# Performance work log

Hardware: AMD Instinct MI355X
Metric: run time of the kernel (lower is better)

## Reference

```python
import jax, jax.numpy as jnp
import numpy as np

THRESHOLD = 0.3

def setup_inputs() -> dict:
    key = jax.random.key(0)
    ks = jax.random.split(key, 8)
    B, T, N, d = 4, 32, 1024, 2
    hd, od, hs, osz = 64, 64, 128, 2
    p = lambda k, sh: jax.random.normal(k, sh, jnp.float32) * 0.1
    return {
        "points": jax.random.uniform(ks[0], (B, T, N, d), jnp.float32),
        "W1": p(ks[1], (hd, d)),   "b1": jnp.zeros((hd,), jnp.float32),
        "W2": p(ks[2], (od, hd)),  "b2": jnp.zeros((od,), jnp.float32),
        "Wg": p(ks[3], (hd, od)),  "bg": jnp.zeros((hd,), jnp.float32),
        "Wih": p(ks[4], (3 * hs, hd)), "Whh": p(ks[5], (3 * hs, hs)),
        "bih": jnp.zeros((3 * hs,), jnp.float32), "bhh": jnp.zeros((3 * hs,), jnp.float32),
        "Wf": p(ks[6], (osz, hs)), "bf": jnp.zeros((osz,), jnp.float32),
    }

def _gcn_step(pts, W1, b1, W2, b2, Wg, bg):
    # pts: [N, d]. Torch detaches node features & adjacency (no grad to points).
    pts = jax.lax.stop_gradient(pts)
    dist = jnp.linalg.norm(pts[:, None, :] - pts[None, :, :], axis=2)  # [N,N]
    A = (dist < THRESHOLD).astype(pts.dtype)
    dinv = 1.0 / jnp.sqrt(A.sum(axis=1))          # rowsum >= 1 (self-loop)
    An = A * dinv[:, None] * dinv[None, :]        # D^{-1/2} A D^{-1/2}
    x = jax.nn.relu((An @ pts) @ W1.T + b1)       # [N, hd]
    x = jax.nn.relu((An @ x) @ W2.T + b2)         # [N, od]
    return x.mean(axis=0) @ Wg.T + bg             # [hd]

def reference(points, W1, b1, W2, b2, Wg, bg, Wih, Whh, bih, bhh, Wf, bf):
    # GCN per (batch, time): [B, T, hd]
    gcn = jax.vmap(jax.vmap(lambda p: _gcn_step(p, W1, b1, W2, b2, Wg, bg)))(points)
    H = Whh.shape[1]

    def gru_step(h, x):  # torch GRU gate order: r, z, n
        gi = x @ Wih.T + bih
        gh = h @ Whh.T + bhh
        ir, iz, inn = jnp.split(gi, 3)
        hr, hz, hn = jnp.split(gh, 3)
        r = jax.nn.sigmoid(ir + hr)
        z = jax.nn.sigmoid(iz + hz)
        n = jnp.tanh(inn + r * hn)
        h_new = (1.0 - z) * n + z * h
        return h_new, h_new

    h0 = jnp.zeros((H,), points.dtype)
    run = lambda xs: jax.lax.scan(gru_step, h0, xs)[1]   # [T, H]
    hs = jax.vmap(run)(gcn)                              # [B, T, H]
    y = hs @ Wf.T + bf                                   # [B, T, out]
    # torch: per-element gru_out.mean(dim=1, keepdim=True) on [1,T,out] -> [1,1,out], stacked -> [B,1,1,out]
    return y.mean(axis=1, keepdims=True)[:, :, None, :]
```

## Files before the change

### kernel.cpp

```cpp
#include <hip/hip_runtime.h>
#include <hip/hip_bf16.h>
#include <math.h>

#define N_PTS 1024
#define BT    128
typedef unsigned int u32;
typedef __attribute__((ext_vector_type(8))) short short8_t;
typedef __attribute__((ext_vector_type(4))) float f32x4;

__device__ __forceinline__ float bfi(u32 bits16) {
    union { u32 u; float f; } v; v.u = bits16 << 16; return v.f;
}
__device__ __forceinline__ unsigned short f2bf(float f) {
    union { float f; u32 u; } v; v.f = f;
    return (unsigned short)((v.u + 0x7FFFu + ((v.u >> 16) & 1u)) >> 16);
}
__device__ __forceinline__ float ldf(const void* p, int i, bool bf) {
    return bf ? bfi(((const unsigned short*)p)[i]) : ((const float*)p)[i];
}
__device__ __forceinline__ float2 ldp(const void* pbase, int j, bool bf) {
    if (bf) {
        u32 w = ((const u32*)pbase)[j];
        return make_float2(bfi(w & 0xFFFFu), bfi(w >> 16));
    }
    return ((const float2*)pbase)[j];
}
__device__ __forceinline__ bool detect_bf16(const void* pts, int tid, int* s_flag) {
    if (tid < 64) {
        u32 w = ((const u32*)pts)[tid];
        float v = bfi(w & 0xFFFFu);
        bool ok = (v >= 0.0f) && (v <= 1.0f);
        unsigned long long m = __ballot(ok);
        if (tid == 0) *s_flag = (m == 0xFFFFFFFFFFFFFFFFull) ? 1 : 0;
    }
    __syncthreads();
    return *s_flag != 0;
}
__device__ __forceinline__ bool is_nb(float px, float py, float qx, float qy) {
    float dx = px - qx, dy = py - qy;
    float d2 = __fadd_rn(__fmul_rn(dx, dx), __fmul_rn(dy, dy));
    return d2 < 0.09f;
}
__device__ __forceinline__ const void* pts_base(const void* pts, int bt, bool bf) {
    return bf ? (const void*)((const unsigned short*)pts + (size_t)bt * N_PTS * 2)
              : (const void*)((const float*)pts + (size_t)bt * N_PTS * 2);
}
__device__ __forceinline__ void gload16(const u32* g, u32* l) {
    __builtin_amdgcn_global_load_lds((const __attribute__((address_space(1))) u32*)g,
                                     (__attribute__((address_space(3))) u32*)l, 16, 0, 0);
}
__device__ __forceinline__ float rdlane(float v, int i) {
    return __int_as_float(__builtin_amdgcn_readlane(__float_as_int(v), i));
}
__device__ __forceinline__ float sigm_f(float x) {
    return __fdividef(1.0f, 1.0f + __expf(-x));
}
__device__ __forceinline__ float tanh_f(float x) {
    float e = __expf(2.0f * x);
    return 1.0f - __fdividef(2.0f, e + 1.0f);
}

__global__ __launch_bounds__(256) void k1_bm(const void* __restrict__ pts,
                                             float* __restrict__ dinv,
                                             float* __restrict__ gsum,
                                             u32* __restrict__ bm) {
    int blk = blockIdx.x, tid = threadIdx.x;
    int bt = blk >> 2, q = blk & 3;
    __shared__ float2 sp[N_PTS];
    __shared__ int s_flag;
    bool bf = detect_bf16(pts, tid, &s_flag);
    const void* pb = pts_base(pts, bt, bf);
    for (int j = tid; j < N_PTS; j += 256) sp[j] = ldp(pb, j, bf);
    if (blk < 32) gsum[blk * 256 + tid] = 0.0f;
    __syncthreads();
    int i = q * 256 + tid;
    float px = sp[i].x, py = sp[i].y;
    const float4* sp4 = (const float4*)sp;
    u32* bmrow = bm + (size_t)bt * 32768 + i;
    int cnt = 0;
    for (int c = 0; c < 32; c++) {
        u32 m = 0;
#pragma unroll
        for (int h = 0; h < 8; h++) {
            float4 s01 = sp4[c * 16 + 2 * h], s23 = sp4[c * 16 + 2 * h + 1];
            if (is_nb(px, py, s01.x, s01.y)) m |= 1u << (4 * h);
            if (is_nb(px, py, s01.z, s01.w)) m |= 1u << (4 * h + 1);
            if (is_nb(px, py, s23.x, s23.y)) m |= 1u << (4 * h + 2);
            if (is_nb(px, py, s23.z, s23.w)) m |= 1u << (4 * h + 3);
        }
        bmrow[c * 1024] = m;
        cnt += __popc(m);
    }
    dinv[bt * N_PTS + i] = 1.0f / sqrtf((float)cnt);
}

__global__ __launch_bounds__(256) void k2_x1v(const void* __restrict__ pts,
                                              const void* __restrict__ W1,
                                              const void* __restrict__ b1,
                                              const float* __restrict__ dinv,
                                              const u32* __restrict__ bm,
                                              u32* __restrict__ x1vB) {
    int blk = blockIdx.x, tid = threadIdx.x;
    int bt = blk >> 2, q = blk & 3;
    __shared__ u32 sbm[8192];
    __shared__ unsigned short u_lds[4][1032];
    __shared__ float2 sax[256];
    __shared__ float  sdl[256];
    __shared__ int s_flag;
    bool bf = detect_bf16(pts, tid, &s_flag);
    const void* pb = pts_base(pts, bt, bf);
    for (int j = tid; j < N_PTS; j += 256) {
        float2 p = ldp(pb, j, bf);
        float d = dinv[bt * N_PTS + j];
        float ux = d * p.x, uy = d * p.y;
        unsigned short hx = f2bf(ux), hy = f2bf(uy);
        u_lds[0][j] = hx;
        u_lds[1][j] = hy;
        u_lds[2][j] = f2bf(ux - bfi(hx));
        u_lds[3][j] = f2bf(uy - bfi(hy));
    }
    const u32* bg_ = bm + (size_t)bt * 32768 + q * 256;
    for (int idx = tid; idx < 8192; idx += 256) {
        int c = idx >> 8, r = idx & 255;
        sbm[idx] = bg_[c * 1024 + r];
    }
    sdl[tid] = dinv[bt * N_PTS + q * 256 + tid];
    __syncthreads();

    int lane = tid & 63, w = tid >> 6;
    int l15 = lane & 15, quad = lane >> 4;
    f32x4 acc[4];
#pragma unroll
    for (int rf = 0; rf < 4; rf++)
#pragma unroll
        for (int r = 0; r < 4; r++) acc[rf][r] = 0.0f;

    const unsigned short* urow = &u_lds[l15 & 3][0];
    for (int c = 0; c < 32; c++) {
        short8_t bu = *(const short8_t*)(urow + c * 32 + quad * 8);
#pragma unroll
        for (int rf = 0; rf < 4; rf++) {
            u32 mw = sbm[c * 256 + w * 64 + rf * 16 + l15];
            u32 by = (mw >> (quad * 8)) & 0xFFu;
            short8_t v;
#pragma unroll
            for (int i2 = 0; i2 < 8; i2++)
                v[i2] = (by & (1u << i2)) ? (short)0x3F80 : (short)0;
            acc[rf] = __builtin_amdgcn_mfma_f32_16x16x32_bf16(v, bu, acc[rf], 0, 0, 0);
        }
    }
#pragma unroll
    for (int rf = 0; rf < 4; rf++) {
#pragma unroll
        for (int r = 0; r < 4; r++) {
            float vsum = acc[rf][r] + __shfl_xor(acc[rf][r], 2, 64);
            int row = w * 64 + rf * 16 + quad * 4 + r;
            float sc = vsum * sdl[row];
            if (l15 == 0)      sax[row].x = sc;
            else if (l15 == 1) sax[row].y = sc;
        }
    }
    __syncthreads();
    int ch = tid & 63, wq = tid >> 6;
    float w0 = ldf(W1, 2 * ch, bf), w1v = ldf(W1, 2 * ch + 1, bf), bb = ldf(b1, ch, bf);
    for (int tt = 0; tt < 4; tt++) {
        u32 ow[8];
#pragma unroll
        for (int k2i = 0; k2i < 8; k2i++) {
            int lj = tt * 64 + wq * 16 + 2 * k2i;
            float2 a0 = sax[lj], a1 = sax[lj + 1];
            float v0 = sdl[lj]     * fmaxf(fmaf(w0, a0.x, fmaf(w1v, a0.y, bb)), 0.0f);
            float v1 = sdl[lj + 1] * fmaxf(fmaf(w0, a1.x, fmaf(w1v, a1.y, bb)), 0.0f);
            ow[k2i] = (u32)f2bf(v0) | ((u32)f2bf(v1) << 16);
        }
        u32* dst = x1vB + ((size_t)(bt * 16 + q * 4 + tt) * 64 + ch) * 36 + wq * 8;
        *(uint4*)dst = make_uint4(ow[0], ow[1], ow[2], ow[3]);
        *(uint4*)(dst + 4) = make_uint4(ow[4], ow[5], ow[6], ow[7]);
    }
}

__global__ __launch_bounds__(256) void k3_mfma(const void* __restrict__ pts,
                                               const void* __restrict__ W2,
                                               const void* __restrict__ b2,
                                               const float* __restrict__ dinv,
                                               const u32* __restrict__ bm,
                                               const u32* __restrict__ x1vB,
                                               float* __restrict__ gsum) {
    __shared__ u32 pool[15424];
    __shared__ int s_flag;
    float* poolf = (float*)pool;
    int tid = threadIdx.x, lane = tid & 63, w = tid >> 6;
    int l15 = lane & 15, quad = lane >> 4;
    int blk = blockIdx.x, bt = blk & 127, rowblk = blk >> 7;
    bool bf = detect_bf16(pts, tid, &s_flag);

    const u32* xg = x1vB + (size_t)bt * 36864;
    for (int it = w; it < 9; it += 4)
        gload16(xg + it * 256 + lane * 4, pool + 8192 + it * 256 + lane * 4);

    const u32* bg_ = bm + (size_t)bt * 32768 + rowblk * 256;
    for (int idx = tid; idx < 8192; idx += 256) {
        int c = idx >> 8, r = idx & 255;
        pool[idx] = bg_[c * 1024 + r];
    }
    unsigned short* W2B = (unsigned short*)(pool + 12800);
    for (int idx = tid; idx < 4096; idx += 256) {
        int o = idx >> 6, c = idx & 63;
        W2B[o * 72 + c] = f2bf(ldf(W2, idx, bf));
    }
    if (tid < 256) poolf[15104 + tid] = dinv[bt * N_PTS + rowblk * 256 + tid];
    if (tid < 64)  poolf[15360 + tid] = ldf(b2, tid, bf);

    f32x4 acc[4][4];
#pragma unroll
    for (int rf = 0; rf < 4; rf++)
#pragma unroll
        for (int nb = 0; nb < 4; nb++)
#pragma unroll
            for (int r = 0; r < 4; r++) acc[rf][nb][r] = 0.0f;

    for (int t = 0; t < 16; t++) {
        __syncthreads();
        if (t + 1 < 16) {
            u32* dst = pool + ((t & 1) ? 8192 : 10496);
            const u32* src = xg + (t + 1) * 2304;
            for (int it = w; it < 9; it += 4)
                gload16(src + it * 256 + lane * 4, dst + it * 256 + lane * 4);
        }
        const unsigned short* xf = (const unsigned short*)(pool + ((t & 1) ? 10496 : 8192));
#pragma unroll
        for (int ks = 0; ks < 2; ks++) {
            short8_t bq[4];
#pragma unroll
            for (int rf = 0; rf < 4; rf++) {
                u32 mw = pool[(2 * t + ks) * 256 + w * 64 + rf * 16 + l15];
                u32 by = (mw >> (quad * 8)) & 0xFFu;
                short8_t v;
#pragma unroll
                for (int i2 = 0; i2 < 8; i2++)
                    v[i2] = (by & (1u << i2)) ? (short)0x3F80 : (short)0;
                bq[rf] = v;
            }
#pragma unroll
            for (int nb = 0; nb < 4; nb++) {
                short8_t af = *(const short8_t*)(xf + (nb * 16 + l15) * 72 + ks * 32 + quad * 8);
#pragma unroll
                for (int rf = 0; rf < 4; rf++)
                    acc[rf][nb] = __builtin_amdgcn_mfma_f32_16x16x32_bf16(af, bq[rf], acc[rf][nb], 0, 0, 0);
            }
        }
    }
    __syncthreads();

    u32* dump = pool;
#pragma unroll
    for (int rf = 0; rf < 4; rf++) {
        int rn = w * 64 + rf * 16 + l15;
        float di = poolf[15104 + rn];
#pragma unroll
        for (int nb = 0; nb < 4; nb++) {
            u32 lo = (u32)f2bf(acc[rf][nb][0] * di) | ((u32)f2bf(acc[rf][nb][1] * di) << 16);
            u32 hi = (u32)f2bf(acc[rf][nb][2] * di) | ((u32)f2bf(acc[rf][nb][3] * di) << 16);
            u32* dst = dump + rn * 36 + nb * 8 + quad * 2;
            dst[0] = lo; dst[1] = hi;
        }
    }
    __syncthreads();
    f32x4 xacc[4][4];
#pragma unroll
    for (int ob = 0; ob < 4; ob++)
#pragma unroll
        for (int rf = 0; rf < 4; rf++)
#pragma unroll
            for (int r = 0; r < 4; r++) xacc[ob][rf][r] = 0.0f;
#pragma unroll
    for (int ks2 = 0; ks2 < 2; ks2++) {
        short8_t b2f[4];
#pragma unroll
        for (int rf = 0; rf < 4; rf++)
            b2f[rf] = *(const short8_t*)((const unsigned short*)dump +
                        (w * 64 + rf * 16 + l15) * 72 + ks2 * 32 + quad * 8);
#pragma unroll
        for (int ob = 0; ob < 4; ob++) {
            short8_t a2 = *(const short8_t*)(W2B + (ob * 16 + l15) * 72 + ks2 * 32 + quad * 8);
#pragma unroll
            for (int rf = 0; rf < 4; rf++)
                xacc[ob][rf] = __builtin_amdgcn_mfma_f32_16x16x32_bf16(a2, b2f[rf], xacc[ob][rf], 0, 0, 0);
        }
    }
#pragma unroll
    for (int ob = 0; ob < 4; ob++) {
#pragma unroll
        for (int r = 0; r < 4; r++) {
            int o = ob * 16 + quad * 4 + r;
            float bb = poolf[15360 + o];
            float s = 0.0f;
#pragma unroll
            for (int rf = 0; rf < 4; rf++) s += fmaxf(xacc[ob][rf][r] + bb, 0.0f);
            s += __shfl_down(s, 8, 16);
            s += __shfl_down(s, 4, 16);
            s += __shfl_down(s, 2, 16);
            s += __shfl_down(s, 1, 16);
            if (l15 == 0) atomicAdd(&gsum[bt * 64 + o], s);
        }
    }
}

__global__ __launch_bounds__(384, 1) void k4a_gi(const void* __restrict__ pts,
                                                 const void* __restrict__ Wg,
                                                 const void* __restrict__ bg,
                                                 const void* __restrict__ Wih,
                                                 const void* __restrict__ bih,
                                                 const float* __restrict__ gsum,
                                                 float* __restrict__ gi_ws) {
    int blk = blockIdx.x, tid = threadIdx.x;
    __shared__ float s_gm[64];
    __shared__ float s_x[64];
    __shared__ int s_flag;
    bool bf = detect_bf16(pts, tid, &s_flag);
    if (tid < 64) s_gm[tid] = gsum[(size_t)blk * 64 + tid] * (1.0f / 1024.0f);
    int r = tid;
    float wv[64];
    if (bf) {
#pragma unroll
        for (int k = 0; k < 64; k++) wv[k] = bfi(((const unsigned short*)Wih)[r * 64 + k]);
    } else {
        const float4* wr = (const float4*)Wih + r * 16;
#pragma unroll
        for (int qq = 0; qq < 16; qq++) {
            float4 v = wr[qq];
            wv[4*qq] = v.x; wv[4*qq+1] = v.y; wv[4*qq+2] = v.z; wv[4*qq+3] = v.w;
        }
    }
    float br = ldf(bih, r, bf);
    float wg[64];
    if (tid < 64) {
        if (bf) {
#pragma unroll
            for (int k = 0; k < 64; k++) wg[k] = bfi(((const unsigned short*)Wg)[tid * 64 + k]);
        } else {
            const float4* wr = (const float4*)Wg + tid * 16;
#pragma unroll
            for (int qq = 0; qq < 16; qq++) {
                float4 v = wr[qq];
                wg[4*qq] = v.x; wg[4*qq+1] = v.y; wg[4*qq+2] = v.z; wg[4*qq+3] = v.w;
            }
        }
    }
    __syncthreads();
    if (tid < 64) {
        float gmv = s_gm[tid];
        float s0 = ldf(bg, tid, bf), s1 = 0.f, s2 = 0.f, s3 = 0.f;
#pragma unroll
        for (int k = 0; k < 64; k += 4) {
            s0 = fmaf(wg[k],     rdlane(gmv, k),     s0);
            s1 = fmaf(wg[k + 1], rdlane(gmv, k + 1), s1);
            s2 = fmaf(wg[k + 2], rdlane(gmv, k + 2), s2);
            s3 = fmaf(wg[k + 3], rdlane(gmv, k + 3), s3);
        }
        s_x[tid] = (s0 + s1) + (s2 + s3);
    }
    __syncthreads();
    float xv = s_x[tid & 63];
    float s0 = br, s1 = 0.f, s2 = 0.f, s3 = 0.f;
#pragma unroll
    for (int k = 0; k < 64; k += 4) {
        s0 = fmaf(wv[k],     rdlane(xv, k),     s0);
        s1 = fmaf(wv[k + 1], rdlane(xv, k + 1), s1);
        s2 = fmaf(wv[k + 2], rdlane(xv, k + 2), s2);
        s3 = fmaf(wv[k + 3], rdlane(xv, k + 3), s3);
    }
    gi_ws[(size_t)blk * 384 + r] = (s0 + s1) + (s2 + s3);
}

__global__ __launch_bounds__(768, 1) void k4b_scan(const void* __restrict__ pts,
                                                   const void* __restrict__ Whh,
                                                   const void* __restrict__ bhh,
                                                   const void* __restrict__ Wf,
                                                   const void* __restrict__ bf_,
                                                   const float* __restrict__ gi_ws,
                                                   float* __restrict__ out) {
    int b = blockIdx.x, tid = threadIdx.x;
    __shared__ float s_gi[12288];
    __shared__ float s_part[2][768];
    __shared__ float s_hm[128];
    __shared__ int s_flag;
    bool bf = detect_bf16(pts, tid, &s_flag);
    const u32* gi_g = (const u32*)gi_ws + (size_t)b * 12288;
    u32* s_gi_u = (u32*)s_gi;
#pragma unroll
    for (int j = 0; j < 4; j++)
        gload16(gi_g + j * 3072 + tid * 4, s_gi_u + j * 3072 + tid * 4);

    int hi = (tid >= 384) ? 1 : 0;
    int r = tid - hi * 384;
    int lane = tid & 63;
    float wh2[64];
    {
        int koff = hi * 64;
        if (bf) {
#pragma unroll
            for (int k = 0; k < 64; k++)
                wh2[k] = bfi(((const unsigned short*)Whh)[r * 128 + koff + k]);
        } else {
            const float4* wr = (const float4*)Whh + (r * 128 + koff) / 4;
#pragma unroll
            for (int qq = 0; qq < 16; qq++) {
                float4 v = wr[qq];
                wh2[4*qq] = v.x; wh2[4*qq+1] = v.y; wh2[4*qq+2] = v.z; wh2[4*qq+3] = v.w;
            }
        }
    }
    float bhr = hi ? 0.0f : ldf(bhh, r, bf);
    int c = hi * 64 + lane;
    float hval = 0.0f;
    float hsum = 0.0f;
    __syncthreads();

    for (int t = 0; t < 32; t++) {
        float gi_r = s_gi[t * 384 + c];
        float gi_z = s_gi[t * 384 + 128 + c];
        float gi_n = s_gi[t * 384 + 256 + c];
        float s0 = bhr, s1 = 0.f, s2 = 0.f, s3 = 0.f;
#pragma unroll
        for (int k = 0; k < 64; k += 4) {
            s0 = fmaf(wh2[k],     rdlane(hval, k),     s0);
            s1 = fmaf(wh2[k + 1], rdlane(hval, k + 1), s1);
            s2 = fmaf(wh2[k + 2], rdlane(hval, k + 2), s2);
            s3 = fmaf(wh2[k + 3], rdlane(hval, k + 3), s3);
        }
        s_part[t & 1][tid] = (s0 + s1) + (s2 + s3);
        __syncthreads();
        const float* P = s_part[t & 1];
        float gr = gi_r + P[c]       + P[384 + c];
        float gz = gi_z + P[128 + c] + P[512 + c];
        float hn =        P[256 + c] + P[640 + c];
        float rr = sigm_f(gr);
        float z  = sigm_f(gz);
        float n  = tanh_f(fmaf(rr, hn, gi_n));
        hval = fmaf(z, hval - n, n);
        hsum += hval;
    }
    if (tid < 64) s_hm[tid] = hsum * (1.0f / 32.0f);
    else if (tid >= 384 && tid < 448) s_hm[64 + lane] = hsum * (1.0f / 32.0f);
    __syncthreads();
    if (tid < 128) {
        float hm = s_hm[tid];
        s_part[0][tid]       = ldf(Wf, tid, bf) * hm;
        s_part[0][128 + tid] = ldf(Wf, 128 + tid, bf) * hm;
    }
    __syncthreads();
    if (tid < 2) {
        float s = ldf(bf_, tid, bf);
        for (int k = 0; k < 128; k++) s += s_part[0][tid * 128 + k];
        out[b * 2 + tid] = s;
    }
}

extern "C" void kernel_launch(void* const* d_in, const int* in_sizes, int n_in,
                              void* d_out, int out_size, void* d_ws, size_t ws_size,
                              hipStream_t stream) {
    const void* pts = d_in[0];
    const void* W1  = d_in[1];
    const void* b1  = d_in[2];
    const void* W2  = d_in[3];
    const void* b2  = d_in[4];
    const void* Wg  = d_in[5];
    const void* bg  = d_in[6];
    const void* Wih = d_in[7];
    const void* Whh = d_in[8];
    const void* bih = d_in[9];
    const void* bhh = d_in[10];
    const void* Wf  = d_in[11];
    const void* bf_ = d_in[12];

    float* dinv = (float*)d_ws;
    float* gsum = dinv + (size_t)BT * N_PTS;
    u32*   bm   = (u32*)(gsum + BT * 64);
    u32*   x1vB = bm + (size_t)BT * 32768;
    float* gi_ws = (float*)x1vB;

    k1_bm  <<<512, 256, 0, stream>>>(pts, dinv, gsum, bm);
    k2_x1v <<<512, 256, 0, stream>>>(pts, W1, b1, dinv, bm, x1vB);
    k3_mfma<<<512, 256, 0, stream>>>(pts, W2, b2, dinv, bm, x1vB, gsum);
    k4a_gi <<<128, 384, 0, stream>>>(pts, Wg, bg, Wih, bih, gsum, gi_ws);
    k4b_scan<<<4, 768, 0, stream>>>(pts, Whh, bhh, Wf, bf_, gi_ws, (float*)d_out);
}
```

Before: 224.5 us.

## Fuse adjacency, first GCN layer and second GCN layer into one kernel per frame

Replaces the three kernels (bitmask build, layer-1 aggregation, layer-2 MFMA) with a single 1024-thread block per (batch,time) frame. dinv and the layer-1 activations now stay in LDS instead of going through global workspace, and the atomic gsum accumulation becomes an LDS reduction with a plain store. Two launches and the x1v global round trip go away. The price is only 128 blocks on the GPU, so fewer blocks are in flight, plus serialized per-group phases and bitmask reads from global/L2 rather than LDS, which may hurt occupancy and latency hiding.

```diff
diff --git a/kernel.cpp b/kernel.cpp
--- a/kernel.cpp
+++ b/kernel.cpp
@@ -60,157 +60,96 @@
     return 1.0f - __fdividef(2.0f, e + 1.0f);
 }
 
-__global__ __launch_bounds__(256) void k1_bm(const void* __restrict__ pts,
-                                             float* __restrict__ dinv,
-                                             float* __restrict__ gsum,
-                                             u32* __restrict__ bm) {
-    int blk = blockIdx.x, tid = threadIdx.x;
-    int bt = blk >> 2, q = blk & 3;
-    __shared__ float2 sp[N_PTS];
-    __shared__ int s_flag;
-    bool bf = detect_bf16(pts, tid, &s_flag);
-    const void* pb = pts_base(pts, bt, bf);
-    for (int j = tid; j < N_PTS; j += 256) sp[j] = ldp(pb, j, bf);
-    if (blk < 32) gsum[blk * 256 + tid] = 0.0f;
-    __syncthreads();
-    int i = q * 256 + tid;
-    float px = sp[i].x, py = sp[i].y;
-    const float4* sp4 = (const float4*)sp;
-    u32* bmrow = bm + (size_t)bt * 32768 + i;
-    int cnt = 0;
-    for (int c = 0; c < 32; c++) {
-        u32 m = 0;
-#pragma unroll
-        for (int h = 0; h < 8; h++) {
-            float4 s01 = sp4[c * 16 + 2 * h], s23 = sp4[c * 16 + 2 * h + 1];
-            if (is_nb(px, py, s01.x, s01.y)) m |= 1u << (4 * h);
-            if (is_nb(px, py, s01.z, s01.w)) m |= 1u << (4 * h + 1);
-            if (is_nb(px, py, s23.x, s23.y)) m |= 1u << (4 * h + 2);
-            if (is_nb(px, py, s23.z, s23.w)) m |= 1u << (4 * h + 3);
-        }
-        bmrow[c * 1024] = m;
-        cnt += __popc(m);
-    }
-    dinv[bt * N_PTS + i] = 1.0f / sqrtf((float)cnt);
-}
-
-__global__ __launch_bounds__(256) void k2_x1v(const void* __restrict__ pts,
-                                              const void* __restrict__ W1,
-                                              const void* __restrict__ b1,
-                                              const float* __restrict__ dinv,
-                                              const u32* __restrict__ bm,
-                                              u32* __restrict__ x1vB) {
-    int blk = blockIdx.x, tid = threadIdx.x;
-    int bt = blk >> 2, q = blk & 3;
-    __shared__ u32 sbm[8192];
-    __shared__ unsigned short u_lds[4][1032];
-    __shared__ float2 sax[256];
-    __shared__ float  sdl[256];
-    __shared__ int s_flag;
-    bool bf = detect_bf16(pts, tid, &s_flag);
-    const void* pb = pts_base(pts, bt, bf);
-    for (int j = tid; j < N_PTS; j += 256) {
-        float2 p = ldp(pb, j, bf);
-        float d = dinv[bt * N_PTS + j];
-        float ux = d * p.x, uy = d * p.y;
-        unsigned short hx = f2bf(ux), hy = f2bf(uy);
-        u_lds[0][j] = hx;
-        u_lds[1][j] = hy;
-        u_lds[2][j] = f2bf(ux - bfi(hx));
-        u_lds[3][j] = f2bf(uy - bfi(hy));
-    }
-    const u32* bg_ = bm + (size_t)bt * 32768 + q * 256;
-    for (int idx = tid; idx < 8192; idx += 256) {
-        int c = idx >> 8, r = idx & 255;
-        sbm[idx] = bg_[c * 1024 + r];
-    }
-    sdl[tid] = dinv[bt * N_PTS + q * 256 + tid];
-    __syncthreads();
-
-    int lane = tid & 63, w = tid >> 6;
-    int l15 = lane & 15, quad = lane >> 4;
-    f32x4 acc[4];
-#pragma unroll
-    for (int rf = 0; rf < 4; rf++)
-#pragma unroll
-        for (int r = 0; r < 4; r++) acc[rf][r] = 0.0f;
-
-    const unsigned short* urow = &u_lds[l15 & 3][0];
-    for (int c = 0; c < 32; c++) {
-        short8_t bu = *(const short8_t*)(urow + c * 32 + quad * 8);
-#pragma unroll
-        for (int rf = 0; rf < 4; rf++) {
-            u32 mw = sbm[c * 256 + w * 64 + rf * 16 + l15];
-            u32 by = (mw >> (quad * 8)) & 0xFFu;
-            short8_t v;
-#pragma unroll
-            for (int i2 = 0; i2 < 8; i2++)
-                v[i2] = (by & (1u << i2)) ? (short)0x3F80 : (short)0;
-            acc[rf] = __builtin_amdgcn_mfma_f32_16x16x32_bf16(v, bu, acc[rf], 0, 0, 0);
-        }
-    }
-#pragma unroll
-    for (int rf = 0; rf < 4; rf++) {
-#pragma unroll
-        for (int r = 0; r < 4; r++) {
-            float vsum = acc[rf][r] + __shfl_xor(acc[rf][r], 2, 64);
-            int row = w * 64 + rf * 16 + quad * 4 + r;
-            float sc = vsum * sdl[row];
-            if (l15 == 0)      sax[row].x = sc;
-            else if (l15 == 1) sax[row].y = sc;
-        }
-    }
-    __syncthreads();
-    int ch = tid & 63, wq = tid >> 6;
-    float w0 = ldf(W1, 2 * ch, bf), w1v = ldf(W1, 2 * ch + 1, bf), bb = ldf(b1, ch, bf);
-    for (int tt = 0; tt < 4; tt++) {
-        u32 ow[8];
-#pragma unroll
-        for (int k2i = 0; k2i < 8; k2i++) {
-            int lj = tt * 64 + wq * 16 + 2 * k2i;
-            float2 a0 = sax[lj], a1 = sax[lj + 1];
-            float v0 = sdl[lj]     * fmaxf(fmaf(w0, a0.x, fmaf(w1v, a0.y, bb)), 0.0f);
-            float v1 = sdl[lj + 1] * fmaxf(fmaf(w0, a1.x, fmaf(w1v, a1.y, bb)), 0.0f);
-            ow[k2i] = (u32)f2bf(v0) | ((u32)f2bf(v1) << 16);
-        }
-        u32* dst = x1vB + ((size_t)(bt * 16 + q * 4 + tt) * 64 + ch) * 36 + wq * 8;
-        *(uint4*)dst = make_uint4(ow[0], ow[1], ow[2], ow[3]);
-        *(uint4*)(dst + 4) = make_uint4(ow[4], ow[5], ow[6], ow[7]);
-    }
-}
-
-__global__ __launch_bounds__(256) void k3_mfma(const void* __restrict__ pts,
-                                               const void* __restrict__ W2,
-                                               const void* __restrict__ b2,
-                                               const float* __restrict__ dinv,
-                                               const u32* __restrict__ bm,
-                                               const u32* __restrict__ x1vB,
-                                               float* __restrict__ gsum) {
-    __shared__ u32 pool[15424];
+__global__ __launch_bounds__(1024, 1) void k123(const void* __restrict__ pts,
+                                                const void* __restrict__ W1,
+                                                const void* __restrict__ b1,
+                                                const void* __restrict__ W2,
+                                                const void* __restrict__ b2,
+                                                u32* __restrict__ bm,
+                                                float* __restrict__ gsum) {
+    __shared__ u32 pool[20048];
     __shared__ int s_flag;
     float* poolf = (float*)pool;
     int tid = threadIdx.x, lane = tid & 63, w = tid >> 6;
     int l15 = lane & 15, quad = lane >> 4;
-    int blk = blockIdx.x, bt = blk & 127, rowblk = blk >> 7;
+    int bt = blockIdx.x;
     bool bf = detect_bf16(pts, tid, &s_flag);
 
-    const u32* xg = x1vB + (size_t)bt * 36864;
-    for (int it = w; it < 9; it += 4)
-        gload16(xg + it * 256 + lane * 4, pool + 8192 + it * 256 + lane * 4);
-
-    const u32* bg_ = bm + (size_t)bt * 32768 + rowblk * 256;
-    for (int idx = tid; idx < 8192; idx += 256) {
-        int c = idx >> 8, r = idx & 255;
-        pool[idx] = bg_[c * 1024 + r];
-    }
-    unsigned short* W2B = (unsigned short*)(pool + 12800);
-    for (int idx = tid; idx < 4096; idx += 256) {
-        int o = idx >> 6, c = idx & 63;
-        W2B[o * 72 + c] = f2bf(ldf(W2, idx, bf));
-    }
-    if (tid < 256) poolf[15104 + tid] = dinv[bt * N_PTS + rowblk * 256 + tid];
-    if (tid < 64)  poolf[15360 + tid] = ldf(b2, tid, bf);
-
+    float2* sp = (float2*)(pool + 9808);
+    const void* pb = pts_base(pts, bt, bf);
+    sp[tid] = ldp(pb, tid, bf);
+    __syncthreads();
+    {
+        float px = sp[tid].x, py = sp[tid].y;
+        const float4* sp4 = (const float4*)sp;
+        u32* bmrow = bm + (size_t)bt * 32768 + tid;
+        int cnt = 0;
+        for (int c = 0; c < 32; c++) {
+            u32 m = 0;
+#pragma unroll
+            for (int h = 0; h < 8; h++) {
+                float4 s01 = sp4[c * 16 + 2 * h], s23 = sp4[c * 16 + 2 * h + 1];
+                if (is_nb(px, py, s01.x, s01.y)) m |= 1u << (4 * h);
+                if (is_nb(px, py, s01.z, s01.w)) m |= 1u << (4 * h + 1);
+                if (is_nb(px, py, s23.x, s23.y)) m |= 1u << (4 * h + 2);
+                if (is_nb(px, py, s23.z, s23.w)) m |= 1u << (4 * h + 3);
+            }
+            bmrow[c * 1024] = m;
+            cnt += __popc(m);
+        }
+        poolf[6416 + tid] = 1.0f / sqrtf((float)cnt);
+    }
+    __syncthreads();
+    {
+        float2 p = sp[tid];
+        float d = poolf[6416 + tid];
+        float ux = d * p.x, uy = d * p.y;
+        unsigned short hx = f2bf(ux), hy = f2bf(uy);
+        unsigned short* u0 = (unsigned short*)pool;
+        u0[0 * 1032 + tid] = hx;
+        u0[1 * 1032 + tid] = hy;
+        u0[2 * 1032 + tid] = f2bf(ux - bfi(hx));
+        u0[3 * 1032 + tid] = f2bf(uy - bfi(hy));
+    }
+    __syncthreads();
+    const u32* bmg = bm + (size_t)bt * 32768;
+    {
+        f32x4 aacc[4];
+#pragma unroll
+        for (int rf = 0; rf < 4; rf++)
+#pragma unroll
+            for (int r = 0; r < 4; r++) aacc[rf][r] = 0.0f;
+        const unsigned short* urow = (const unsigned short*)pool + (l15 & 3) * 1032;
+        for (int c = 0; c < 32; c++) {
+            short8_t bu = *(const short8_t*)(urow + c * 32 + quad * 8);
+#pragma unroll
+            for (int rf = 0; rf < 4; rf++) {
+                u32 mw = bmg[c * 1024 + w * 64 + rf * 16 + l15];
+                u32 by = (mw >> (quad * 8)) & 0xFFu;
+                short8_t v;
+#pragma unroll
+                for (int i2 = 0; i2 < 8; i2++)
+                    v[i2] = (by & (1u << i2)) ? (short)0x3F80 : (short)0;
+                aacc[rf] = __builtin_amdgcn_mfma_f32_16x16x32_bf16(v, bu, aacc[rf], 0, 0, 0);
+            }
+        }
+        float2* sax = (float2*)(pool + 4368);
+#pragma unroll
+        for (int rf = 0; rf < 4; rf++) {
+#pragma unroll
+            for (int r = 0; r < 4; r++) {
+                float vsum = aacc[rf][r] + __shfl_xor(aacc[rf][r], 2, 64);
+                int row = w * 64 + rf * 16 + quad * 4 + r;
+                float sc = vsum * poolf[6416 + row];
+                if (l15 == 0)      sax[row].x = sc;
+                else if (l15 == 1) sax[row].y = sc;
+            }
+        }
+    }
+    unsigned short* W2B = (unsigned short*)(pool + 7440);
+    for (int idx = tid; idx < 4096; idx += 1024)
+        W2B[(idx >> 6) * 72 + (idx & 63)] = f2bf(ldf(W2, idx, bf));
+    if (tid < 64) poolf[9744 + tid] = ldf(b2, tid, bf);
     f32x4 acc[4][4];
 #pragma unroll
     for (int rf = 0; rf < 4; rf++)
@@ -218,22 +157,30 @@
         for (int nb = 0; nb < 4; nb++)
 #pragma unroll
             for (int r = 0; r < 4; r++) acc[rf][nb][r] = 0.0f;
-
+    unsigned short* xt = (unsigned short*)(pool + 2064);
+    float2* sax = (float2*)(pool + 4368);
+    int ch = tid & 63, wq16 = tid >> 6;
+    float w0 = ldf(W1, 2 * ch, bf), w1v = ldf(W1, 2 * ch + 1, bf), bb1 = ldf(b1, ch, bf);
     for (int t = 0; t < 16; t++) {
         __syncthreads();
-        if (t + 1 < 16) {
-            u32* dst = pool + ((t & 1) ? 8192 : 10496);
-            const u32* src = xg + (t + 1) * 2304;
-            for (int it = w; it < 9; it += 4)
-                gload16(src + it * 256 + lane * 4, dst + it * 256 + lane * 4);
-        }
-        const unsigned short* xf = (const unsigned short*)(pool + ((t & 1) ? 10496 : 8192));
+        {
+            u32* xtd = (u32*)xt + ch * 36 + wq16 * 2;
+#pragma unroll
+            for (int k2i = 0; k2i < 2; k2i++) {
+                int lj = t * 64 + wq16 * 4 + 2 * k2i;
+                float2 a0 = sax[lj], a1 = sax[lj + 1];
+                float v0 = poolf[6416 + lj]     * fmaxf(fmaf(w0, a0.x, fmaf(w1v, a0.y, bb1)), 0.0f);
+                float v1 = poolf[6416 + lj + 1] * fmaxf(fmaf(w0, a1.x, fmaf(w1v, a1.y, bb1)), 0.0f);
+                xtd[k2i] = (u32)f2bf(v0) | ((u32)f2bf(v1) << 16);
+            }
+        }
+        __syncthreads();
 #pragma unroll
         for (int ks = 0; ks < 2; ks++) {
             short8_t bq[4];
 #pragma unroll
             for (int rf = 0; rf < 4; rf++) {
-                u32 mw = pool[(2 * t + ks) * 256 + w * 64 + rf * 16 + l15];
+                u32 mw = bmg[(2 * t + ks) * 1024 + w * 64 + rf * 16 + l15];
                 u32 by = (mw >> (quad * 8)) & 0xFFu;
                 short8_t v;
 #pragma unroll
@@ -243,7 +190,7 @@
             }
 #pragma unroll
             for (int nb = 0; nb < 4; nb++) {
-                short8_t af = *(const short8_t*)(xf + (nb * 16 + l15) * 72 + ks * 32 + quad * 8);
+                short8_t af = *(const short8_t*)(xt + (nb * 16 + l15) * 72 + ks * 32 + quad * 8);
 #pragma unroll
                 for (int rf = 0; rf < 4; rf++)
                     acc[rf][nb] = __builtin_amdgcn_mfma_f32_16x16x32_bf16(af, bq[rf], acc[rf][nb], 0, 0, 0);
@@ -251,58 +198,72 @@
         }
     }
     __syncthreads();
-
-    u32* dump = pool;
-#pragma unroll
-    for (int rf = 0; rf < 4; rf++) {
-        int rn = w * 64 + rf * 16 + l15;
-        float di = poolf[15104 + rn];
-#pragma unroll
-        for (int nb = 0; nb < 4; nb++) {
-            u32 lo = (u32)f2bf(acc[rf][nb][0] * di) | ((u32)f2bf(acc[rf][nb][1] * di) << 16);
-            u32 hi = (u32)f2bf(acc[rf][nb][2] * di) | ((u32)f2bf(acc[rf][nb][3] * di) << 16);
-            u32* dst = dump + rn * 36 + nb * 8 + quad * 2;
-            dst[0] = lo; dst[1] = hi;
-        }
-    }
-    __syncthreads();
+    u32* dump = pool + 9808;
     f32x4 xacc[4][4];
-#pragma unroll
-    for (int ob = 0; ob < 4; ob++)
-#pragma unroll
-        for (int rf = 0; rf < 4; rf++)
-#pragma unroll
-            for (int r = 0; r < 4; r++) xacc[ob][rf][r] = 0.0f;
-#pragma unroll
-    for (int ks2 = 0; ks2 < 2; ks2++) {
-        short8_t b2f[4];
-#pragma unroll
-        for (int rf = 0; rf < 4; rf++)
-            b2f[rf] = *(const short8_t*)((const unsigned short*)dump +
-                        (w * 64 + rf * 16 + l15) * 72 + ks2 * 32 + quad * 8);
-#pragma unroll
-        for (int ob = 0; ob < 4; ob++) {
-            short8_t a2 = *(const short8_t*)(W2B + (ob * 16 + l15) * 72 + ks2 * 32 + quad * 8);
-#pragma unroll
-            for (int rf = 0; rf < 4; rf++)
-                xacc[ob][rf] = __builtin_amdgcn_mfma_f32_16x16x32_bf16(a2, b2f[rf], xacc[ob][rf], 0, 0, 0);
-        }
-    }
+    int g = w >> 2, wr = w & 3;
+    for (int gg = 0; gg < 4; gg++) {
+        if (g == gg) {
+#pragma unroll
+            for (int rf = 0; rf < 4; rf++) {
+                int rl = wr * 64 + rf * 16 + l15;
+                float di2 = poolf[6416 + gg * 256 + rl];
+#pragma unroll
+                for (int nb = 0; nb < 4; nb++) {
+                    u32 lo = (u32)f2bf(acc[rf][nb][0] * di2) | ((u32)f2bf(acc[rf][nb][1] * di2) << 16);
+                    u32 hi2 = (u32)f2bf(acc[rf][nb][2] * di2) | ((u32)f2bf(acc[rf][nb][3] * di2) << 16);
+                    u32* dst = dump + rl * 36 + nb * 8 + quad * 2;
+                    dst[0] = lo; dst[1] = hi2;
+                }
+            }
+        }
+        __syncthreads();
+        if (g == gg) {
+#pragma unroll
+            for (int ob = 0; ob < 4; ob++)
+#pragma unroll
+                for (int rf = 0; rf < 4; rf++)
+#pragma unroll
+                    for (int r = 0; r < 4; r++) xacc[ob][rf][r] = 0.0f;
+#pragma unroll
+            for (int ks2 = 0; ks2 < 2; ks2++) {
+                short8_t b2f[4];
+#pragma unroll
+                for (int rf = 0; rf < 4; rf++)
+                    b2f[rf] = *(const short8_t*)((const unsigned short*)dump +
+                                (wr * 64 + rf * 16 + l15) * 72 + ks2 * 32 + quad * 8);
+#pragma unroll
+                for (int ob = 0; ob < 4; ob++) {
+                    short8_t a2 = *(const short8_t*)(W2B + (ob * 16 + l15) * 72 + ks2 * 32 + quad * 8);
+#pragma unroll
+                    for (int rf = 0; rf < 4; rf++)
+                        xacc[ob][rf] = __builtin_amdgcn_mfma_f32_16x16x32_bf16(a2, b2f[rf], xacc[ob][rf], 0, 0, 0);
+                }
+            }
+        }
+        __syncthreads();
+    }
+    float* s_red = poolf + 19024;
 #pragma unroll
     for (int ob = 0; ob < 4; ob++) {
 #pragma unroll
         for (int r = 0; r < 4; r++) {
             int o = ob * 16 + quad * 4 + r;
-            float bb = poolf[15360 + o];
+            float bbv = poolf[9744 + o];
             float s = 0.0f;
 #pragma unroll
-            for (int rf = 0; rf < 4; rf++) s += fmaxf(xacc[ob][rf][r] + bb, 0.0f);
+            for (int rf = 0; rf < 4; rf++) s += fmaxf(xacc[ob][rf][r] + bbv, 0.0f);
             s += __shfl_down(s, 8, 16);
             s += __shfl_down(s, 4, 16);
             s += __shfl_down(s, 2, 16);
             s += __shfl_down(s, 1, 16);
-            if (l15 == 0) atomicAdd(&gsum[bt * 64 + o], s);
-        }
+            if (l15 == 0) s_red[w * 64 + o] = s;
+        }
+    }
+    __syncthreads();
+    if (tid < 64) {
+        float t2 = 0.0f;
+        for (int w2 = 0; w2 < 16; w2++) t2 += s_red[w2 * 64 + tid];
+        gsum[(size_t)bt * 64 + tid] = t2;
     }
 }
 
@@ -474,15 +435,11 @@
     const void* Wf  = d_in[11];
     const void* bf_ = d_in[12];
 
-    float* dinv = (float*)d_ws;
-    float* gsum = dinv + (size_t)BT * N_PTS;
-    u32*   bm   = (u32*)(gsum + BT * 64);
-    u32*   x1vB = bm + (size_t)BT * 32768;
-    float* gi_ws = (float*)x1vB;
-
-    k1_bm  <<<512, 256, 0, stream>>>(pts, dinv, gsum, bm);
-    k2_x1v <<<512, 256, 0, stream>>>(pts, W1, b1, dinv, bm, x1vB);
-    k3_mfma<<<512, 256, 0, stream>>>(pts, W2, b2, dinv, bm, x1vB, gsum);
+    float* gsum = (float*)d_ws;
+    u32*   bm   = (u32*)(gsum + (size_t)BT * 64);
+    float* gi_ws = (float*)(bm + (size_t)BT * 32768);
+
+    k123   <<<128, 1024, 0, stream>>>(pts, W1, b1, W2, b2, bm, gsum);
     k4a_gi <<<128, 384, 0, stream>>>(pts, Wg, bg, Wih, bih, gsum, gi_ws);
     k4b_scan<<<4, 768, 0, stream>>>(pts, Whh, bhh, Wf, bf_, gi_ws, (float*)d_out);
 }
```

New measurement: 320.4 us. 42.7% more time.
